# Performance work log

Hardware: AMD Instinct MI355X
Metric: run time of the kernel (lower is better)

Reference implementation:

```python
import jax, jax.numpy as jnp
import numpy as np

B, T, I = 256, 512, 256
H = 256  # hidden_dim == input_dim (required by zeros_like(seq[0]))


def setup_inputs() -> dict:
    key = jax.random.key(0)
    k1, k2, k3 = jax.random.split(key, 3)
    bound = 1.0 / np.sqrt(I + H)  # torch nn.Linear default init
    inputs = jax.random.normal(k1, (B, T, I), dtype=jnp.float32)
    W = jax.random.uniform(k2, (4 * H, I + H), minval=-bound, maxval=bound, dtype=jnp.float32)
    b = jax.random.uniform(k3, (4 * H,), minval=-bound, maxval=bound, dtype=jnp.float32)
    return {"inputs": inputs, "W": W, "b": b}


def reference(inputs, W, b):
    # inputs: [B, T, I]; W: [4H, I+H]; b: [4H]
    hidden0 = jnp.zeros((inputs.shape[0], H), dtype=inputs.dtype)
    cell0 = jnp.zeros((inputs.shape[0], H), dtype=inputs.dtype)

    def step(carry, x_t):
        hidden, cell = carry
        catted = jnp.concatenate([x_t, hidden], axis=-1)  # [B, I+H]
        res = catted @ W.T + b                            # [B, 4H]
        i, j, f, o = jnp.split(res, 4, axis=1)
        ai = jax.nn.sigmoid(i)
        af = jax.nn.sigmoid(f)
        ao = jax.nn.sigmoid(o)
        aj = jnp.tanh(j)
        next_c = ai * aj + cell * af
        next_h = ao * jnp.tanh(next_c)
        return (next_h, next_c), None

    xs = jnp.swapaxes(inputs, 0, 1)  # [T, B, I] for scan over time
    (hidden, cell), _ = jax.lax.scan(step, (hidden0, cell0), xs)
    return hidden
```

## Files before the change

### kernel.cpp

```cpp
#include <hip/hip_runtime.h>
#include <hip/hip_bf16.h>
#include <stdint.h>

namespace {

constexpr int Tn = 512, In = 256, Hn = 256, Kn = 512;

typedef __attribute__((ext_vector_type(8))) short bf16x8;
typedef __attribute__((ext_vector_type(4))) float f32x4;
typedef __attribute__((ext_vector_type(4))) unsigned int u32x4;

__device__ __forceinline__ float sigmoidf_(float x) { return 1.f / (1.f + __expf(-x)); }
__device__ __forceinline__ float tanhf_(float x)    { return 2.f / (1.f + __expf(-2.f * x)) - 1.f; }

__device__ __forceinline__ int swz(int c) { return c ^ ((c >> 4) & 15); }
__device__ __forceinline__ int swz16(int c) { return c ^ (((c >> 3) & 3) << 1); }

__device__ __forceinline__ void bar_lds() {
    asm volatile("s_waitcnt lgkmcnt(0)\n\ts_barrier" ::: "memory");
}

__device__ __forceinline__ void st16_llc(void* p, bf16x8 v) {
    asm volatile("global_store_dwordx4 %0, %1, off sc1" :: "v"(p), "v"(v) : "memory");
}
__device__ __forceinline__ bf16x8 ld16_llc(const void* p) {
    bf16x8 r;
    asm volatile("global_load_dwordx4 %0, %1, off sc1" : "=v"(r) : "v"(p) : "memory");
    return r;
}
__device__ __forceinline__ u32x4 ld16u_llc(const void* p) {
    u32x4 r;
    asm volatile("global_load_dwordx4 %0, %1, off sc1" : "=v"(r) : "v"(p) : "memory");
    return r;
}
__device__ __forceinline__ u32x4 ldflags_llc(const void* p) {
    u32x4 r;
    asm volatile("global_load_dwordx4 %0, %1, off sc1\n\ts_waitcnt vmcnt(0)"
                 : "=v"(r) : "v"(p) : "memory");
    return r;
}
__device__ __forceinline__ void stdw_llc(void* p, uint32_t v) {
    asm volatile("global_store_dword %0, %1, off sc1" :: "v"(p), "v"(v) : "memory");
}

__device__ __forceinline__ bool tags8(u32x4 a, u32x4 b, uint32_t wt) {
    uint32_t d = (a.x ^ wt) | (a.y ^ wt) | (a.z ^ wt) | (a.w ^ wt)
               | (b.x ^ wt) | (b.y ^ wt) | (b.z ^ wt) | (b.w ^ wt);
    return (d & 0xFFFF0000u) == 0u;
}
__device__ __forceinline__ bf16x8 pack8(u32x4 a, u32x4 b) {
    union { uint32_t u[4]; bf16x8 v; } r;
    r.u[0] = (a.x & 0xFFFFu) | (a.y << 16);
    r.u[1] = (a.z & 0xFFFFu) | (a.w << 16);
    r.u[2] = (b.x & 0xFFFFu) | (b.y << 16);
    r.u[3] = (b.z & 0xFFFFu) | (b.w << 16);
    return r.v;
}


__global__ void pack_w_tag(const float* __restrict__ W, __hip_bfloat16* __restrict__ Wpf,
                           unsigned long long* __restrict__ hz) {
    int idx  = blockIdx.x * 256 + threadIdx.x;
    int lane = idx & 63;
    int kb   = (idx >> 6) & 15;
    int nt2  = idx >> 10;
    int g = nt2 & 3, wu = (nt2 >> 2) & 3, jj = nt2 >> 4;
    int row = g * 256 + jj * 64 + wu * 16 + (lane & 15);
    int k0  = kb * 32 + (lane >> 4) * 8;
    const float* src = W + (size_t)row * Kn + k0;
    union { __hip_bfloat16 h[8]; bf16x8 v; } u;
#pragma unroll
    for (int e = 0; e < 8; ++e) u.h[e] = __float2bfloat16(src[e]);
    *(bf16x8*)(Wpf + (size_t)idx * 8) = u.v;
    hz[idx] = 0ULL;
}

__global__ __launch_bounds__(512, 2) void lstm_tag(
    const float* __restrict__ X, const float* __restrict__ bias,
    const __hip_bfloat16* __restrict__ Wpf, char* __restrict__ hbuf,
    float* __restrict__ out)
{
    __shared__ bf16x8 AfrX[2][512];
    __shared__ bf16x8 AfrH[512];
    __shared__ f32x4 Red[4][4][64];

    const int tid = threadIdx.x, lane = tid & 63, w8 = tid >> 6;
    const int wu = w8 & 3, ks = w8 >> 2;
    const int l15 = lane & 15, lk = lane >> 4;
    const int wg = blockIdx.x, cl = wg & 15, j = wg >> 4;

    bf16x8 wf[4][8];
#pragma unroll
    for (int g = 0; g < 4; ++g)
#pragma unroll
        for (int i = 0; i < 8; ++i) {
            const int nt2 = (j * 4 + wu) * 4 + g, kb = ks * 8 + i;
            wf[g][i] = *(const bf16x8*)(Wpf + ((size_t)(nt2 * 16 + kb) * 64 + lane) * 8);
        }
    float bg[4];
#pragma unroll
    for (int g = 0; g < 4; ++g) bg[g] = bias[g * 256 + j * 64 + wu * 16 + l15];

    float c4[4] = {0.f, 0.f, 0.f, 0.f};

    {
        const bf16x8 z = {};
        AfrH[tid] = z;
    }

    const int b = wu * 4 + lk;
    const float* xbase = X + (size_t)(cl * 16 + b) * Tn * In;
    float4 xp[4];
    if (ks == 0) {
#pragma unroll
        for (int cc = 0; cc < 2; ++cc) {
            const int o8 = l15 + cc * 16;
            const float4 v0 = *(const float4*)(xbase + o8 * 8);
            const float4 v1 = *(const float4*)(xbase + o8 * 8 + 4);
            union { __hip_bfloat16 h[8]; bf16x8 v; } u;
            u.h[0] = __float2bfloat16(v0.x); u.h[1] = __float2bfloat16(v0.y);
            u.h[2] = __float2bfloat16(v0.z); u.h[3] = __float2bfloat16(v0.w);
            u.h[4] = __float2bfloat16(v1.x); u.h[5] = __float2bfloat16(v1.y);
            u.h[6] = __float2bfloat16(v1.z); u.h[7] = __float2bfloat16(v1.w);
            AfrX[0][swz(b + 16 * o8)] = u.v;
        }
#pragma unroll
        for (int cc = 0; cc < 2; ++cc) {
            const int o8 = l15 + cc * 16;
            xp[cc * 2]     = *(const float4*)(xbase + In + o8 * 8);
            xp[cc * 2 + 1] = *(const float4*)(xbase + In + o8 * 8 + 4);
        }
    }
    __syncthreads();

#pragma unroll 1
    for (int t = 0; t < Tn; ++t) {
        if (ks == 0) {
            f32x4 acc[4] = {};
            bf16x8 af[8];
#pragma unroll
            for (int i = 0; i < 8; ++i)
                af[i] = AfrX[t & 1][swz(i * 64 + lane)];
#pragma unroll
            for (int i = 0; i < 8; ++i)
#pragma unroll
                for (int g = 0; g < 4; ++g)
                    acc[g] = __builtin_amdgcn_mfma_f32_16x16x32_bf16(af[i], wf[g][i], acc[g], 0, 0, 0);
#pragma unroll
            for (int g = 0; g < 4; ++g) Red[wu][g][lane] = acc[g];
            if (t + 1 < Tn) {
#pragma unroll
                for (int cc = 0; cc < 2; ++cc) {
                    const int o8 = l15 + cc * 16;
                    union { __hip_bfloat16 h[8]; bf16x8 v; } u;
                    u.h[0] = __float2bfloat16(xp[cc * 2].x); u.h[1] = __float2bfloat16(xp[cc * 2].y);
                    u.h[2] = __float2bfloat16(xp[cc * 2].z); u.h[3] = __float2bfloat16(xp[cc * 2].w);
                    u.h[4] = __float2bfloat16(xp[cc * 2 + 1].x); u.h[5] = __float2bfloat16(xp[cc * 2 + 1].y);
                    u.h[6] = __float2bfloat16(xp[cc * 2 + 1].z); u.h[7] = __float2bfloat16(xp[cc * 2 + 1].w);
                    AfrX[(t + 1) & 1][swz(b + 16 * o8)] = u.v;
                }
            }
        } else if (t > 0 && wu != j) {
            const char* ib = hbuf + (size_t)(((cl * 4 + wu) * 2 + (t & 1)) * 4096)
                           + (lane & 15) * 256 + (lane >> 4) * 32;
            const uint32_t wt = ((uint32_t)t) << 16;
            u32x4 A0 = {}, A1 = {}, B0 = {}, B1 = {};
            bool f0 = false, f1 = false;
            int g2 = 0;
            for (;;) {
                if (!f0) { A0 = ld16u_llc(ib);       A1 = ld16u_llc(ib + 16); }
                if (!f1) { B0 = ld16u_llc(ib + 128); B1 = ld16u_llc(ib + 144); }
                asm volatile("s_waitcnt vmcnt(0)" ::: "memory");
                f0 = f0 || tags8(A0, A1, wt);
                f1 = f1 || tags8(B0, B1, wt);
                if (__all(f0 && f1) || ++g2 >= 1024) break;
            }
            __builtin_amdgcn_sched_barrier(0);
            AfrH[swz(wu * 128 + lane)]      = pack8(A0, A1);
            AfrH[swz(wu * 128 + 64 + lane)] = pack8(B0, B1);
        }
        bar_lds();

        uint16_t hb[4];
        if (ks == 0) {
            if (t + 2 < Tn) {
                const float* xs = xbase + (size_t)(t + 2) * In;
#pragma unroll
                for (int cc = 0; cc < 2; ++cc) {
                    const int o8 = l15 + cc * 16;
                    xp[cc * 2]     = *(const float4*)(xs + o8 * 8);
                    xp[cc * 2 + 1] = *(const float4*)(xs + o8 * 8 + 4);
                }
            }
        } else {
            f32x4 acc[4] = {};
            bf16x8 af[8];
#pragma unroll
            for (int i = 0; i < 8; ++i)
                af[i] = AfrH[swz(i * 64 + lane)];
#pragma unroll
            for (int i = 0; i < 8; ++i)
#pragma unroll
                for (int g = 0; g < 4; ++g)
                    acc[g] = __builtin_amdgcn_mfma_f32_16x16x32_bf16(af[i], wf[g][i], acc[g], 0, 0, 0);
#pragma unroll
            for (int g = 0; g < 4; ++g) acc[g] += Red[wu][g][lane];
#pragma unroll
            for (int r = 0; r < 4; ++r) {
                const float pi = acc[0][r] + bg[0];
                const float pj = acc[1][r] + bg[1];
                const float pf = acc[2][r] + bg[2];
                const float po = acc[3][r] + bg[3];
                const float ai = sigmoidf_(pi);
                const float aj = tanhf_(pj);
                const float afv = sigmoidf_(pf);
                const float ao = sigmoidf_(po);
                const float cn = ai * aj + c4[r] * afv;
                c4[r] = cn;
                const float hn = ao * tanhf_(cn);
                if (t < Tn - 1) {
                    union { __hip_bfloat16 bh; uint16_t u; } cv;
                    cv.bh = __float2bfloat16(hn);
                    hb[r] = cv.u;
                } else {
                    out[(size_t)(cl * 16 + lk * 4 + r) * Hn + j * 64 + wu * 16 + l15] = hn;
                }
            }
            if (t < Tn - 1) {
                asm volatile("s_waitcnt vmcnt(0)" ::: "memory");
                char* eb = hbuf + (size_t)(((cl * 4 + j) * 2 + ((t + 1) & 1)) * 4096);
                const uint32_t tagw = ((uint32_t)(t + 1)) << 16;
#pragma unroll
                for (int r = 0; r < 4; ++r)
                    stdw_llc(eb + (((lk * 4 + r) * 64 + wu * 16 + l15) << 2),
                             (uint32_t)hb[r] | tagw);
            }
        }
        bar_lds();

        if (ks == 1 && t < Tn - 1) {
#pragma unroll
            for (int r = 0; r < 4; ++r) {
                const int c = j * 128 + (wu >> 1) * 64
                            + ((wu & 1) * 2 + (l15 >> 3)) * 16 + lk * 4 + r;
                *(uint16_t*)((char*)AfrH + swz(c) * 16 + (l15 & 7) * 2) = hb[r];
            }
        }
    }
}

__global__ void pack_w_frag(const float* __restrict__ W, __hip_bfloat16* __restrict__ Wpf,
                            uint32_t* __restrict__ flags) {
    int idx  = blockIdx.x * 256 + threadIdx.x;
    int lane = idx & 63;
    int kb   = (idx >> 6) & 15;
    int nt2  = idx >> 10;
    int g = nt2 & 3, wu = (nt2 >> 2) & 3, jj = nt2 >> 4;
    int row = g * 256 + jj * 64 + wu * 16 + (lane & 15);
    int k0  = kb * 32 + (lane >> 4) * 8;
    const float* src = W + (size_t)row * Kn + k0;
    union { __hip_bfloat16 h[8]; bf16x8 v; } u;
#pragma unroll
    for (int e = 0; e < 8; ++e) u.h[e] = __float2bfloat16(src[e]);
    *(bf16x8*)(Wpf + (size_t)idx * 8) = u.v;
    if (blockIdx.x == 0 && threadIdx.x < 256)
        flags[threadIdx.x] = 0u;
}

__global__ __launch_bounds__(512, 2) void lstm_cluster(
    const float* __restrict__ X, const float* __restrict__ bias,
    const __hip_bfloat16* __restrict__ Wpf, __hip_bfloat16* __restrict__ hbuf,
    uint32_t* __restrict__ flags, float* __restrict__ out)
{
    __shared__ bf16x8 AfrX[2][512];
    __shared__ bf16x8 AfrH[512];
    __shared__ f32x4 Red[4][4][64];
    __shared__ bf16x8 Tp[4][32];

    const int tid = threadIdx.x, lane = tid & 63, w8 = tid >> 6;
    const int wu = w8 & 3, ks = w8 >> 2;
    const int l15 = lane & 15, lk = lane >> 4;
    const int wg = blockIdx.x, cl = wg & 15, j = wg >> 4;

    bf16x8 wf[4][8];
#pragma unroll
    for (int g = 0; g < 4; ++g)
#pragma unroll
        for (int i = 0; i < 8; ++i) {
            const int nt2 = (j * 4 + wu) * 4 + g, kb = ks * 8 + i;
            wf[g][i] = *(const bf16x8*)(Wpf + ((size_t)(nt2 * 16 + kb) * 64 + lane) * 8);
        }
    float bg[4];
#pragma unroll
    for (int g = 0; g < 4; ++g) bg[g] = bias[g * 256 + j * 64 + wu * 16 + l15];
    float c4[4] = {0.f, 0.f, 0.f, 0.f};
    {
        const bf16x8 z = {};
        AfrH[tid] = z;
    }
    const int b = wu * 4 + lk;
    const float* xbase = X + (size_t)(cl * 16 + b) * Tn * In;
    float4 xp[4];
    if (ks == 0) {
#pragma unroll
        for (int cc = 0; cc < 2; ++cc) {
            const int o8 = l15 + cc * 16;
            const float4 v0 = *(const float4*)(xbase + o8 * 8);
            const float4 v1 = *(const float4*)(xbase + o8 * 8 + 4);
            union { __hip_bfloat16 h[8]; bf16x8 v; } u;
            u.h[0] = __float2bfloat16(v0.x); u.h[1] = __float2bfloat16(v0.y);
            u.h[2] = __float2bfloat16(v0.z); u.h[3] = __float2bfloat16(v0.w);
            u.h[4] = __float2bfloat16(v1.x); u.h[5] = __float2bfloat16(v1.y);
            u.h[6] = __float2bfloat16(v1.z); u.h[7] = __float2bfloat16(v1.w);
            AfrX[0][swz(b + 16 * o8)] = u.v;
        }
#pragma unroll
        for (int cc = 0; cc < 2; ++cc) {
            const int o8 = l15 + cc * 16;
            xp[cc * 2]     = *(const float4*)(xbase + In + o8 * 8);
            xp[cc * 2 + 1] = *(const float4*)(xbase + In + o8 * 8 + 4);
        }
    }
    __syncthreads();
#pragma unroll 1
    for (int t = 0; t < Tn; ++t) {
        f32x4 acc[4] = {};
        if (ks == 0) {
            bf16x8 af[8];
#pragma unroll
            for (int i = 0; i < 8; ++i)
                af[i] = AfrX[t & 1][swz(i * 64 + lane)];
#pragma unroll
            for (int i = 0; i < 8; ++i)
#pragma unroll
                for (int g = 0; g < 4; ++g)
                    acc[g] = __builtin_amdgcn_mfma_f32_16x16x32_bf16(af[i], wf[g][i], acc[g], 0, 0, 0);
            if (t + 1 < Tn) {
#pragma unroll
                for (int cc = 0; cc < 2; ++cc) {
                    const int o8 = l15 + cc * 16;
                    union { __hip_bfloat16 h[8]; bf16x8 v; } u;
                    u.h[0] = __float2bfloat16(xp[cc * 2].x); u.h[1] = __float2bfloat16(xp[cc * 2].y);
                    u.h[2] = __float2bfloat16(xp[cc * 2].z); u.h[3] = __float2bfloat16(xp[cc * 2].w);
                    u.h[4] = __float2bfloat16(xp[cc * 2 + 1].x); u.h[5] = __float2bfloat16(xp[cc * 2 + 1].y);
                    u.h[6] = __float2bfloat16(xp[cc * 2 + 1].z); u.h[7] = __float2bfloat16(xp[cc * 2 + 1].w);
                    AfrX[(t + 1) & 1][swz(b + 16 * o8)] = u.v;
                }
            }
        } else if (t > 0 && wu != j) {
            const char* fl = (const char*)flags + (cl * 4 + wu) * 16;
            uint32_t g2 = 0;
            for (;;) {
                u32x4 f = ldflags_llc(fl);
                uint32_t mn = f.x < f.y ? f.x : f.y;
                const uint32_t mn2 = f.z < f.w ? f.z : f.w;
                if (mn2 < mn) mn = mn2;
                if (mn >= (uint32_t)t || ++g2 >= (1u << 12)) break;
            }
            const char* src = (const char*)hbuf + (size_t)((t & 1) * 16 + cl) * 8192
                            + wu * 2048 + lane * 16;
            const bf16x8 r0 = ld16_llc(src);
            const bf16x8 r1 = ld16_llc(src + 1024);
            asm volatile("s_waitcnt vmcnt(0)" ::: "memory");
            __builtin_amdgcn_sched_barrier(0);
            AfrH[swz(wu * 128 + lane)]      = r0;
            AfrH[swz(wu * 128 + lane + 64)] = r1;
        }
        __syncthreads();
        if (ks == 0) {
            if (t + 2 < Tn) {
                const float* xs = xbase + (size_t)(t + 2) * In;
#pragma unroll
                for (int cc = 0; cc < 2; ++cc) {
                    const int o8 = l15 + cc * 16;
                    xp[cc * 2]     = *(const float4*)(xs + o8 * 8);
                    xp[cc * 2 + 1] = *(const float4*)(xs + o8 * 8 + 4);
                }
            }
        } else {
            bf16x8 af[8];
#pragma unroll
            for (int i = 0; i < 8; ++i)
                af[i] = AfrH[swz(i * 64 + lane)];
#pragma unroll
            for (int i = 0; i < 8; ++i)
#pragma unroll
                for (int g = 0; g < 4; ++g)
                    acc[g] = __builtin_amdgcn_mfma_f32_16x16x32_bf16(af[i], wf[g][i], acc[g], 0, 0, 0);
#pragma unroll
            for (int g = 0; g < 4; ++g) Red[wu][g][lane] = acc[g];
        }
        __syncthreads();
        if (ks == 0) {
#pragma unroll
            for (int g = 0; g < 4; ++g) acc[g] += Red[wu][g][lane];
            __hip_bfloat16* tp = (__hip_bfloat16*)&Tp[wu][0];
#pragma unroll
            for (int r = 0; r < 4; ++r) {
                const float pi = acc[0][r] + bg[0];
                const float pj = acc[1][r] + bg[1];
                const float pf = acc[2][r] + bg[2];
                const float po = acc[3][r] + bg[3];
                const float ai = sigmoidf_(pi);
                const float aj = tanhf_(pj);
                const float afv = sigmoidf_(pf);
                const float ao = sigmoidf_(po);
                const float cn = ai * aj + c4[r] * afv;
                c4[r] = cn;
                const float hn = ao * tanhf_(cn);
                if (t < Tn - 1) {
                    const int cp = (lk * 4 + r) * 2 + (l15 >> 3);
                    tp[swz16(cp) * 8 + (l15 & 7)] = __float2bfloat16(hn);
                } else {
                    out[(size_t)(cl * 16 + lk * 4 + r) * Hn + j * 64 + wu * 16 + l15] = hn;
                }
            }
            if (t < Tn - 1) {
                if (lane < 32) {
                    const bf16x8 val = Tp[wu][swz16(lane)];
                    const int clocal = (wu >> 1) * 64 + (lane >> 1)
                                     + 16 * ((wu & 1) * 2 + (lane & 1));
                    AfrH[swz(j * 128 + clocal)] = val;
                    char* dst = (char*)hbuf + (size_t)(((t + 1) & 1) * 16 + cl) * 8192
                              + j * 2048 + clocal * 16;
                    st16_llc(dst, val);
                }
                asm volatile("s_waitcnt vmcnt(0)" ::: "memory");
                if (lane == 0)
                    stdw_llc((char*)flags + (cl * 4 + j) * 16 + wu * 4, (uint32_t)(t + 1));
            }
        }
    }
}

__global__ void pack_w(const float* __restrict__ W, __hip_bfloat16* __restrict__ Wp) {
    int idx = blockIdx.x * 256 + threadIdx.x;
    int e = idx & 7, l = (idx >> 3) & 63, kb = (idx >> 9) & 15, nt = idx >> 13;
    int n = nt * 16 + (l & 15);
    int k = kb * 32 + (l >> 4) * 8 + e;
    Wp[idx] = __float2bfloat16(W[n * Kn + k]);
}

__global__ __launch_bounds__(1024, 4) void lstm_fused(
    const float* __restrict__ X, const float* __restrict__ bias,
    const __hip_bfloat16* __restrict__ Wp, float* __restrict__ out)
{
    constexpr int LDA = Kn + 8;
    __shared__ __hip_bfloat16 A[16][LDA];
    const int tid = threadIdx.x, wv = tid >> 6, lane = tid & 63;
    const int l15 = lane & 15, lk = lane >> 4, b0 = blockIdx.x * 16;
    const __hip_bfloat16* wp[4];
#pragma unroll
    for (int g = 0; g < 4; ++g) wp[g] = Wp + (size_t)(g * 16 + wv) * (16 * 512) + lane * 8;
    float bslot[4];
#pragma unroll
    for (int g = 0; g < 4; ++g) bslot[g] = bias[g * 256 + wv * 16 + l15];
    float c[4], h[4];
#pragma unroll
    for (int r = 0; r < 4; ++r) { c[r] = 0.f; h[r] = 0.f; }
    const float* xptr = X + ((size_t)(b0 + wv) * Tn) * In + lane * 4;
#pragma unroll 1
    for (int t = 0; t < Tn; ++t) {
        __syncthreads();
        {
            const float4 v = *(const float4*)(xptr + (size_t)t * In);
            __hip_bfloat16 tmp[4];
            tmp[0] = __float2bfloat16(v.x); tmp[1] = __float2bfloat16(v.y);
            tmp[2] = __float2bfloat16(v.z); tmp[3] = __float2bfloat16(v.w);
            *(ushort4*)&A[wv][lane * 4] = *(const ushort4*)tmp;
        }
#pragma unroll
        for (int r = 0; r < 4; ++r)
            A[lk * 4 + r][In + wv * 16 + l15] = __float2bfloat16(h[r]);
        __syncthreads();
        f32x4 acc[4];
#pragma unroll
        for (int g = 0; g < 4; ++g) acc[g] = f32x4{bslot[g], bslot[g], bslot[g], bslot[g]};
        bf16x8 wbuf[2][4];
#pragma unroll
        for (int g = 0; g < 4; ++g) wbuf[0][g] = *(const bf16x8*)(wp[g]);
#pragma unroll
        for (int kb = 0; kb < 16; ++kb) {
            const int cur = kb & 1;
            if (kb < 15) {
#pragma unroll
                for (int g = 0; g < 4; ++g)
                    wbuf[cur ^ 1][g] = *(const bf16x8*)(wp[g] + (kb + 1) * 512);
            }
            const bf16x8 a = *(const bf16x8*)&A[l15][kb * 32 + lk * 8];
#pragma unroll
            for (int g = 0; g < 4; ++g)
                acc[g] = __builtin_amdgcn_mfma_f32_16x16x32_bf16(a, wbuf[cur][g], acc[g], 0, 0, 0);
        }
#pragma unroll
        for (int r = 0; r < 4; ++r) {
            const float ai = sigmoidf_(acc[0][r]);
            const float aj = tanhf_(acc[1][r]);
            const float af = sigmoidf_(acc[2][r]);
            const float ao = sigmoidf_(acc[3][r]);
            const float cn = ai * aj + c[r] * af;
            c[r] = cn;
            h[r] = ao * tanhf_(cn);
            if (t == Tn - 1)
                out[(size_t)(b0 + lk * 4 + r) * Hn + wv * 16 + l15] = h[r];
        }
    }
}

}

extern "C" void kernel_launch(void* const* d_in, const int* in_sizes, int n_in,
                              void* d_out, int out_size, void* d_ws, size_t ws_size,
                              hipStream_t stream) {
    const float* X    = (const float*)d_in[0];
    const float* W    = (const float*)d_in[1];
    const float* bias = (const float*)d_in[2];

    if (ws_size >= (size_t)0x180000) {
        __hip_bfloat16* Wpf = (__hip_bfloat16*)d_ws;
        char*           hb  = (char*)d_ws + 0x100000;
        pack_w_tag<<<dim3(256), dim3(256), 0, stream>>>(W, Wpf, (unsigned long long*)hb);
        lstm_tag<<<dim3(64), dim3(512), 0, stream>>>(X, bias, Wpf, hb, (float*)d_out);
    } else if (ws_size >= (size_t)0x142000) {
        __hip_bfloat16* Wpf   = (__hip_bfloat16*)d_ws;
        __hip_bfloat16* hbuf  = (__hip_bfloat16*)((char*)d_ws + 0x100000);
        uint32_t*       flags = (uint32_t*)((char*)d_ws + 0x140000);
        pack_w_frag<<<dim3(256), dim3(256), 0, stream>>>(W, Wpf, flags);
        lstm_cluster<<<dim3(64), dim3(512), 0, stream>>>(X, bias, Wpf, hbuf, flags,
                                                         (float*)d_out);
    } else {
        __hip_bfloat16* Wp = (__hip_bfloat16*)d_ws;
        pack_w<<<dim3(2048), dim3(256), 0, stream>>>(W, Wp);
        lstm_fused<<<dim3(16), dim3(1024), 0, stream>>>(X, bias, Wp, (float*)d_out);
    }
}
```

Baseline: 1.108 ms.

## Assign LSTM cluster roles by XCD so exchange stays in local L2

Launches 256 workgroups that report their hardware XCC ID. Workgroup 0 then groups four blocks that share an XCD into each of the 16 batch clusters, and the surplus blocks exit. Because every cluster now sits on one XCD, hidden-state exchange stores and polling loads use sc0 (L2 scope) instead of sc1 (LLC), with an occasional sc1 fallback and a longer spin limit. This is meant to cut inter-workgroup communication latency per time step. It relies on co-residency and spin-waiting for the role table, uses the output buffer as scratch for that table, and risks deadlock or stale data if a cluster does not land on one XCD.

```diff
diff --git a/kernel.cpp b/kernel.cpp
--- a/kernel.cpp
+++ b/kernel.cpp
@@ -25,11 +25,6 @@
 }
 __device__ __forceinline__ bf16x8 ld16_llc(const void* p) {
     bf16x8 r;
-    asm volatile("global_load_dwordx4 %0, %1, off sc1" : "=v"(r) : "v"(p) : "memory");
-    return r;
-}
-__device__ __forceinline__ u32x4 ld16u_llc(const void* p) {
-    u32x4 r;
     asm volatile("global_load_dwordx4 %0, %1, off sc1" : "=v"(r) : "v"(p) : "memory");
     return r;
 }
@@ -41,6 +36,21 @@
 }
 __device__ __forceinline__ void stdw_llc(void* p, uint32_t v) {
     asm volatile("global_store_dword %0, %1, off sc1" :: "v"(p), "v"(v) : "memory");
+}
+__device__ __forceinline__ uint32_t lddw_llc(const void* p) {
+    uint32_t r;
+    asm volatile("global_load_dword %0, %1, off sc1\n\ts_waitcnt vmcnt(0)"
+                 : "=v"(r) : "v"(p) : "memory");
+    return r;
+}
+__device__ __forceinline__ void stdw_l2(void* p, uint32_t v) {
+    asm volatile("global_store_dword %0, %1, off sc0" :: "v"(p), "v"(v) : "memory");
+}
+__device__ __forceinline__ u32x4 ld16u_s(const void* p, bool llc) {
+    u32x4 r;
+    if (llc) asm volatile("global_load_dwordx4 %0, %1, off sc1" : "=v"(r) : "v"(p) : "memory");
+    else     asm volatile("global_load_dwordx4 %0, %1, off sc0" : "=v"(r) : "v"(p) : "memory");
+    return r;
 }
 
 __device__ __forceinline__ bool tags8(u32x4 a, u32x4 b, uint32_t wt) {
@@ -59,7 +69,7 @@
 
 
 __global__ void pack_w_tag(const float* __restrict__ W, __hip_bfloat16* __restrict__ Wpf,
-                           unsigned long long* __restrict__ hz) {
+                           unsigned long long* __restrict__ hz, uint32_t* __restrict__ tab) {
     int idx  = blockIdx.x * 256 + threadIdx.x;
     int lane = idx & 63;
     int kb   = (idx >> 6) & 15;
@@ -73,21 +83,87 @@
     for (int e = 0; e < 8; ++e) u.h[e] = __float2bfloat16(src[e]);
     *(bf16x8*)(Wpf + (size_t)idx * 8) = u.v;
     hz[idx] = 0ULL;
-}
-
-__global__ __launch_bounds__(512, 2) void lstm_tag(
+    if (blockIdx.x == 0 && threadIdx.x < 256) {
+        tab[threadIdx.x] = 0u;
+        tab[256 + threadIdx.x] = 0u;
+    }
+}
+
+__global__ __launch_bounds__(512, 2) void lstm_xcd(
     const float* __restrict__ X, const float* __restrict__ bias,
     const __hip_bfloat16* __restrict__ Wpf, char* __restrict__ hbuf,
-    float* __restrict__ out)
+    uint32_t* __restrict__ tab, float* __restrict__ out)
 {
     __shared__ bf16x8 AfrX[2][512];
     __shared__ bf16x8 AfrH[512];
     __shared__ f32x4 Red[4][4][64];
+    __shared__ uint32_t roleSh;
 
     const int tid = threadIdx.x, lane = tid & 63, w8 = tid >> 6;
     const int wu = w8 & 3, ks = w8 >> 2;
     const int l15 = lane & 15, lk = lane >> 4;
-    const int wg = blockIdx.x, cl = wg & 15, j = wg >> 4;
+    const int wg = blockIdx.x;
+
+    uint32_t* xcdtab = tab;
+    uint32_t* asgn   = tab + 256;
+
+    uint32_t xcc;
+    asm volatile("s_getreg_b32 %0, hwreg(HW_REG_XCC_ID)" : "=s"(xcc));
+    if (tid == 0) {
+        uint32_t v = (xcc & 7) + 1;
+        asm volatile("global_store_dword %0, %1, off sc1\n\ts_waitcnt vmcnt(0)"
+                     :: "v"(xcdtab + wg), "v"(v) : "memory");
+    }
+
+    if (wg == 0) {
+        uint32_t* xtabL = (uint32_t*)&AfrX[0][0];
+        uint32_t* asgnL = xtabL + 256;
+        if (tid < 256) {
+            uint32_t v = 0;
+            for (uint32_t g2 = 0; g2 < (1u << 16); ++g2) {
+                v = lddw_llc(xcdtab + tid);
+                if (v != 0) break;
+            }
+            xtabL[tid] = v;
+            asgnL[tid] = 1u;
+        }
+        __syncthreads();
+        if (tid == 0) {
+            int cnt[8] = {0, 0, 0, 0, 0, 0, 0, 0};
+            int pend[8][4];
+            int ncl = 0;
+            for (int i = 0; i < 256 && ncl < 16; ++i) {
+                const int x = (int)((xtabL[i] - 1u) & 7u);
+                pend[x][cnt[x] & 3] = i;
+                cnt[x]++;
+                if ((cnt[x] & 3) == 0) {
+                    for (int m = 0; m < 4; ++m)
+                        asgnL[pend[x][m]] = 2u + (uint32_t)(ncl * 4 + m);
+                    ncl++;
+                }
+            }
+        }
+        __syncthreads();
+        if (tid < 256)
+            asm volatile("global_store_dword %0, %1, off sc1"
+                         :: "v"(asgn + tid), "v"(asgnL[tid]) : "memory");
+        asm volatile("s_waitcnt vmcnt(0)" ::: "memory");
+    }
+
+    if (tid == 0) {
+        uint32_t v = 0;
+        for (uint32_t g2 = 0; g2 < (1u << 20); ++g2) {
+            v = lddw_llc(asgn + wg);
+            if (v != 0) break;
+        }
+        roleSh = v;
+    }
+    __syncthreads();
+    const uint32_t role = roleSh;
+    if (role < 2u) return;
+    const int slot = (int)(role - 2u);
+    const int cl = slot >> 2, j = slot & 3;
+    __syncthreads();
 
     bf16x8 wf[4][8];
 #pragma unroll
@@ -168,12 +244,13 @@
             bool f0 = false, f1 = false;
             int g2 = 0;
             for (;;) {
-                if (!f0) { A0 = ld16u_llc(ib);       A1 = ld16u_llc(ib + 16); }
-                if (!f1) { B0 = ld16u_llc(ib + 128); B1 = ld16u_llc(ib + 144); }
+                const bool llc = ((g2 & 15) >= 12);
+                if (!f0) { A0 = ld16u_s(ib, llc);       A1 = ld16u_s(ib + 16, llc); }
+                if (!f1) { B0 = ld16u_s(ib + 128, llc); B1 = ld16u_s(ib + 144, llc); }
                 asm volatile("s_waitcnt vmcnt(0)" ::: "memory");
                 f0 = f0 || tags8(A0, A1, wt);
                 f1 = f1 || tags8(B0, B1, wt);
-                if (__all(f0 && f1) || ++g2 >= 1024) break;
+                if (__all(f0 && f1) || ++g2 >= 4096) break;
             }
             __builtin_amdgcn_sched_barrier(0);
             AfrH[swz(wu * 128 + lane)]      = pack8(A0, A1);
@@ -232,8 +309,8 @@
                 const uint32_t tagw = ((uint32_t)(t + 1)) << 16;
 #pragma unroll
                 for (int r = 0; r < 4; ++r)
-                    stdw_llc(eb + (((lk * 4 + r) * 64 + wu * 16 + l15) << 2),
-                             (uint32_t)hb[r] | tagw);
+                    stdw_l2(eb + (((lk * 4 + r) * 64 + wu * 16 + l15) << 2),
+                            (uint32_t)hb[r] | tagw);
             }
         }
         bar_lds();
@@ -519,8 +596,9 @@
     if (ws_size >= (size_t)0x180000) {
         __hip_bfloat16* Wpf = (__hip_bfloat16*)d_ws;
         char*           hb  = (char*)d_ws + 0x100000;
-        pack_w_tag<<<dim3(256), dim3(256), 0, stream>>>(W, Wpf, (unsigned long long*)hb);
-        lstm_tag<<<dim3(64), dim3(512), 0, stream>>>(X, bias, Wpf, hb, (float*)d_out);
+        uint32_t*       tab = (uint32_t*)d_out;
+        pack_w_tag<<<dim3(256), dim3(256), 0, stream>>>(W, Wpf, (unsigned long long*)hb, tab);
+        lstm_xcd<<<dim3(256), dim3(512), 0, stream>>>(X, bias, Wpf, hb, tab, (float*)d_out);
     } else if (ws_size >= (size_t)0x142000) {
         __hip_bfloat16* Wpf   = (__hip_bfloat16*)d_ws;
         __hip_bfloat16* hbuf  = (__hip_bfloat16*)((char*)d_ws + 0x100000);
```

Measured after the change: 2.316 ms. +109.1%, slower.
